# Optimization experiments

Measured on AMD Instinct MI355X. Metric: run time of the kernel, lower is better.

Reference implementation:

```python
import jax, jax.numpy as jnp
import numpy as np

PI_APPROX = 3.14  # the original module uses 3.14, not math.pi
FPS = 30.0        # hard-coded sampling rate in calc_hr_torch


def setup_inputs() -> dict:
    key = jax.random.key(0)
    x = jax.random.normal(key, (4096, 4096), dtype=jnp.float32)
    return {"x": x}


def reference(x) -> jnp.ndarray:
    test_n, sig_length = x.shape
    # mean-subtract each signal (over last dim)
    x = x - jnp.mean(x, axis=-1, keepdims=True)

    # custom_fft: DFT over dim 0 (size test_n), O(N^2) via trig matmuls
    N = test_n
    n = jnp.arange(N, dtype=jnp.float32)[:, None]  # [N,1]
    k = jnp.arange(N, dtype=jnp.float32)[None, :]  # [1,N]
    ang = (-2.0 * PI_APPROX / N) * (k * n)         # [N,N]
    real_part = jnp.matmul(jnp.cos(ang), x)        # [N, sig_length]
    imag_part = jnp.matmul(jnp.sin(ang), x)

    # custom_rfft: keep non-negative frequencies along dim 0
    half = N // 2 + 1 if N % 2 == 0 else (N + 1) // 2
    real_part = real_part[:half]
    imag_part = imag_part[:half]

    Ns = sig_length
    freq = jnp.arange(Ns, dtype=jnp.float32) / (Ns / FPS)  # [sig_length]
    amplitude = jnp.sqrt(real_part ** 2 + imag_part ** 2) / Ns  # [half, sig_length]
    hr_list = freq[jnp.argmax(amplitude, axis=-1)] * 60.0       # [half]
    return hr_list
```

## Files before the change

kernel.cpp:

```cpp
#include <hip/hip_runtime.h>
#include <cmath>

typedef _Float16 f16;
typedef _Float16 f16x8 __attribute__((ext_vector_type(8)));
typedef float f32x4 __attribute__((ext_vector_type(4)));
typedef unsigned long long u64;

#define M_OUT 2049
#define NDIM 4096
#define MPAD 2112
#define CW ((float)(-2.0 * 3.14 / 4096.0))

static const size_t WS_MEAN  = 0;
static const size_t WS_CELLS = 16384;
static const size_t WS_TBL   = 40960;
static const size_t A_ELEMS  = (size_t)MPAD * NDIM;
static const size_t X_ELEMS  = (size_t)NDIM * NDIM;
static const size_t WS_XTBL  = WS_TBL + 4 * A_ELEMS * sizeof(f16);
static const size_t WS_FULL_END = WS_XTBL + 2 * X_ELEMS * sizeof(f16);
static const size_t WS_MID_END  = WS_TBL + 4 * A_ELEMS * sizeof(f16);

#define AS1 __attribute__((address_space(1)))
#define AS3 __attribute__((address_space(3)))
__device__ __forceinline__ void async_copy16(const void* gsrc, void* ldst) {
    __builtin_amdgcn_global_load_lds((const AS1 unsigned int*)gsrc,
                                     (AS3 unsigned int*)ldst, 16, 0, 0);
}

__device__ __forceinline__ void split_f16(float v, f16& hi, f16& lo) {
    hi = (f16)v;
    lo = (f16)((v - (float)hi) * 64.0f);
}
__device__ __forceinline__ void split_raw(float v, f16& hi, f16& lo) {
    hi = (f16)v;
    lo = (f16)(v - (float)hi);
}

__global__ void mean_kernel(const float* __restrict__ x, float* __restrict__ meanv,
                            u64* __restrict__ cells) {
    if (blockIdx.x < 9) {
        int i = blockIdx.x * 256 + threadIdx.x;
        if (i < M_OUT) cells[i] = 0ull;
    }
    const int row = blockIdx.x;
    const float4* xr = (const float4*)(x + (size_t)row * NDIM);
    float s = 0.f;
    for (int i = threadIdx.x; i < NDIM / 4; i += 256) {
        float4 v = xr[i];
        s += (v.x + v.y) + (v.z + v.w);
    }
    for (int off = 32; off; off >>= 1) s += __shfl_down(s, off);
    __shared__ float ps[4];
    if ((threadIdx.x & 63) == 0) ps[threadIdx.x >> 6] = s;
    __syncthreads();
    if (threadIdx.x == 0) {
        float t = (ps[0] + ps[1]) + (ps[2] + ps[3]);
        meanv[row] = t * (1.0f / 4096.0f);
    }
}

__global__ __launch_bounds__(256) void nyq_partial(
    const float* __restrict__ x, const float* __restrict__ meanv,
    float* __restrict__ part)
{
    __shared__ float lc[256], ls[256];
    __shared__ float sC[128], sS[128];
    const int t = threadIdx.x;
    const int ks = blockIdx.y;
    const int kbase = ks * 256;
    sincosf(CW * (float)(2048 * (kbase + t)), &ls[t], &lc[t]);
    __syncthreads();
    const int col = blockIdx.x * 128 + (t & 127);
    const int kp  = t >> 7;
    float C = 0.f, S = 0.f;
    const float* xp = x + (size_t)(kbase + kp * 128) * NDIM + col;
    const float* mp = meanv + kbase + kp * 128;
    for (int i = 0; i < 128; ++i) {
        float v = xp[(size_t)i * NDIM] - mp[i];
        C = fmaf(lc[kp * 128 + i], v, C);
        S = fmaf(ls[kp * 128 + i], v, S);
    }
    if (kp) { sC[t - 128] = C; sS[t - 128] = S; }
    __syncthreads();
    if (!kp) {
        part[(size_t)ks * NDIM + col]            = C + sC[t];
        part[(size_t)(16 + ks) * NDIM + col]     = S + sS[t];
    }
}

__global__ __launch_bounds__(256) void nyq_reduce(
    const float* __restrict__ part, u64* __restrict__ cells)
{
    const int n = blockIdx.x * 256 + threadIdx.x;
    float C = 0.f, S = 0.f;
    for (int ks = 0; ks < 16; ++ks) {
        C += part[(size_t)ks * NDIM + n];
        S += part[(size_t)(16 + ks) * NDIM + n];
    }
    float a2 = C * C + S * S;
    u64 key = ((u64)__float_as_uint(a2) << 32) | (unsigned)(~n);
    for (int off = 1; off < 64; off <<= 1) {
        unsigned hi = (unsigned)(key >> 32), lo = (unsigned)key;
        unsigned ho = __shfl_xor(hi, off), lo2 = __shfl_xor(lo, off);
        u64 o = ((u64)ho << 32) | lo2;
        if (o > key) key = o;
    }
    if ((threadIdx.x & 63) == 0) atomicMax(cells + 2048, key);
}

__global__ void fill_tables_cm(const float* __restrict__ x, const float* __restrict__ meanv,
                               f16* __restrict__ atbl, f16* __restrict__ xtbl) {
    const int c = blockIdx.x;
    if (blockIdx.y < 9) {
        const int m = blockIdx.y * 256 + threadIdx.x;
        if (m >= MPAD) return;
        const bool valid = (m < M_OUT);
        f16x8 chv, clv, shv, slv;
        for (int j = 0; j < 8; ++j) {
            float cc = 0.f, ss = 0.f;
            if (valid) {
                int kk = c * 8 + j;
                float ang = CW * (float)(m * kk);
                sincosf(ang, &ss, &cc);
            }
            f16 h, l;
            split_raw(cc, h, l); chv[j] = h; clv[j] = l;
            split_raw(ss, h, l); shv[j] = h; slv[j] = l;
        }
        size_t idx = ((size_t)c * MPAD + m) * 8;
        *(f16x8*)(atbl + idx)                 = chv;
        *(f16x8*)(atbl + A_ELEMS + idx)       = clv;
        *(f16x8*)(atbl + 2 * A_ELEMS + idx)   = shv;
        *(f16x8*)(atbl + 3 * A_ELEMS + idx)   = slv;
    } else {
        const int n = (blockIdx.y - 9) * 256 + threadIdx.x;
        f16x8 hv, lv;
        for (int j = 0; j < 8; ++j) {
            int k = c * 8 + j;
            float v = x[(size_t)k * NDIM + n] - meanv[k];
            f16 h, l;
            split_raw(v, h, l);
            hv[j] = h; lv[j] = l;
        }
        size_t idx = ((size_t)c * NDIM + n) * 8;
        *(f16x8*)(xtbl + idx)           = hv;
        *(f16x8*)(xtbl + X_ELEMS + idx) = lv;
    }
}

__global__ __launch_bounds__(256, 4) void dft_gemm_cm(
    const f16* __restrict__ atbl, const f16* __restrict__ xtbl,
    u64* __restrict__ cells)
{
    __shared__ alignas(16) f16 sX[2][2][4][128][8];

    const int t = threadIdx.x;
    const int n0      = blockIdx.x * 128;
    const int rowBase = blockIdx.y * 64;

    const int lane = t & 63;
    const int w  = t >> 6;
    const int wm = w >> 1, wn = w & 1;
    const int q  = lane >> 4, ln = lane & 15;

    f32x4 aC[2][4], aS[2][4];
#pragma unroll
    for (int i = 0; i < 2; ++i)
#pragma unroll
        for (int j = 0; j < 4; ++j) {
            aC[i][j] = (f32x4){0.f, 0.f, 0.f, 0.f};
            aS[i][j] = (f32x4){0.f, 0.f, 0.f, 0.f};
        }

    const f16* aBase = atbl + ((size_t)q * MPAD + (rowBase + wm * 32 + ln)) * 8;

    const int xq0 = w >> 1, xh = w & 1;
    const int xq1 = xq0 + 2;
    const f16* xG0 = xtbl + ((size_t)xq0 * NDIM + n0 + xh * 64 + lane) * 8;
    const f16* xG1 = xtbl + ((size_t)xq1 * NDIM + n0 + xh * 64 + lane) * 8;
    const f16* xG2 = xG0 + X_ELEMS;
    const f16* xG3 = xG1 + X_ELEMS;

    auto loadA = [&](f16x8 (&dst)[2][4], int kc) {
#pragma unroll
        for (int tm = 0; tm < 2; ++tm)
#pragma unroll
            for (int tb = 0; tb < 4; ++tb)
                dst[tm][tb] = *(const f16x8*)(aBase + (size_t)tb * A_ELEMS
                              + ((size_t)kc * MPAD + tm * 16) * 8);
    };

    auto stageX = [&](int buf, int kc) {
        const size_t kadv = (size_t)kc * NDIM * 8;
        async_copy16(xG0 + kadv, &sX[buf][0][xq0][xh * 64][0]);
        async_copy16(xG1 + kadv, &sX[buf][0][xq1][xh * 64][0]);
        async_copy16(xG2 + kadv, &sX[buf][1][xq0][xh * 64][0]);
        async_copy16(xG3 + kadv, &sX[buf][1][xq1][xh * 64][0]);
    };

    auto compute = [&](f16x8 (&A)[2][4], int buf) {
        f16x8 bh[4], bl[4];
#pragma unroll
        for (int tn = 0; tn < 4; ++tn) {
            int nl = wn * 64 + tn * 16 + ln;
            bh[tn] = *(const f16x8*)&sX[buf][0][q][nl][0];
            bl[tn] = *(const f16x8*)&sX[buf][1][q][nl][0];
        }
        __builtin_amdgcn_s_setprio(1);
#pragma unroll
        for (int tm = 0; tm < 2; ++tm)
#pragma unroll
            for (int tn = 0; tn < 4; ++tn) {
                aC[tm][tn] = __builtin_amdgcn_mfma_f32_16x16x32_f16(A[tm][0], bh[tn], aC[tm][tn], 0, 0, 0);
                aC[tm][tn] = __builtin_amdgcn_mfma_f32_16x16x32_f16(A[tm][0], bl[tn], aC[tm][tn], 0, 0, 0);
                aC[tm][tn] = __builtin_amdgcn_mfma_f32_16x16x32_f16(A[tm][1], bh[tn], aC[tm][tn], 0, 0, 0);
                aS[tm][tn] = __builtin_amdgcn_mfma_f32_16x16x32_f16(A[tm][2], bh[tn], aS[tm][tn], 0, 0, 0);
                aS[tm][tn] = __builtin_amdgcn_mfma_f32_16x16x32_f16(A[tm][2], bl[tn], aS[tm][tn], 0, 0, 0);
                aS[tm][tn] = __builtin_amdgcn_mfma_f32_16x16x32_f16(A[tm][3], bh[tn], aS[tm][tn], 0, 0, 0);
            }
        __builtin_amdgcn_s_setprio(0);
    };

    f16x8 Aa[2][4];
    int cur = 0;

    stageX(0, 0);

    for (int kc = 0; kc < 512; kc += 4) {
        __syncthreads();
        if (kc + 4 < 512) stageX(cur ^ 1, kc + 4);
        loadA(Aa, kc);
        compute(Aa, cur);
        cur ^= 1;
    }

#pragma unroll
    for (int tm = 0; tm < 2; ++tm) {
#pragma unroll
        for (int r = 0; r < 4; ++r) {
            u64 best = 0ull;
#pragma unroll
            for (int tn = 0; tn < 4; ++tn) {
                float C = aC[tm][tn][r];
                float S = aS[tm][tn][r];
                float a2 = C * C + S * S;
                int col = n0 + wn * 64 + tn * 16 + ln;
                u64 key = ((u64)__float_as_uint(a2) << 32) | (unsigned)(~col);
                if (key > best) best = key;
            }
            for (int off = 1; off < 16; off <<= 1) {
                unsigned hi = (unsigned)(best >> 32), lo = (unsigned)best;
                unsigned ho = __shfl_xor(hi, off);
                unsigned lo2 = __shfl_xor(lo, off);
                u64 o = ((u64)ho << 32) | lo2;
                if (o > best) best = o;
            }
            if (ln == 0) {
                int grow = rowBase + wm * 32 + tm * 16 + q * 4 + r;
                if (grow < M_OUT) atomicMax(cells + grow, best);
            }
        }
    }
}

__global__ void fill_tables_rm(f16* __restrict__ tbl) {
    long long g = (long long)blockIdx.x * 256 + threadIdx.x;
    if (g >= (long long)(MPAD * 512)) return;
    int m  = (int)(g >> 9);
    int kq = ((int)g & 511) * 8;
    bool valid = (m < M_OUT);
    f16x8 chv, clv, shv, slv;
    for (int j = 0; j < 8; ++j) {
        float c = 0.f, s = 0.f;
        if (valid) {
            int kk = kq + j;
            float ang = CW * (float)(m * kk);
            sincosf(ang, &s, &c);
        }
        f16 h, l;
        split_f16(c, h, l); chv[j] = h; clv[j] = l;
        split_f16(s, h, l); shv[j] = h; slv[j] = l;
    }
    size_t idx = (size_t)m * NDIM + kq;
    *(f16x8*)(tbl + idx)               = chv;
    *(f16x8*)(tbl + A_ELEMS + idx)     = clv;
    *(f16x8*)(tbl + 2 * A_ELEMS + idx) = shv;
    *(f16x8*)(tbl + 3 * A_ELEMS + idx) = slv;
}

#define PK 40
__global__ __launch_bounds__(256, 2) void dft_gemm_fb(
    const float* __restrict__ x, const float* __restrict__ meanv,
    const f16* __restrict__ tbl, int useTbl,
    u64* __restrict__ cells)
{
    __shared__ alignas(16) f16 Ach[64][PK];
    __shared__ alignas(16) f16 Acl[64][PK];
    __shared__ alignas(16) f16 Ash[64][PK];
    __shared__ alignas(16) f16 Asl[64][PK];
    __shared__ alignas(16) f16 Xh[128][PK];
    __shared__ alignas(16) f16 Xl[128][PK];

    const int t = threadIdx.x;
    const int n0      = blockIdx.x * 128;
    const int rowBase = blockIdx.y * 64;

    const int am  = t >> 2;
    const int akq = (t & 3) * 8;
    const int xn  = t & 127;
    const int xkh = (t >> 7) * 16;

    const int lane = t & 63;
    const int w  = t >> 6;
    const int wm = w >> 1, wn = w & 1;
    const int q  = lane >> 4, ln = lane & 15;

    f32x4 aC0[2][4], aC1[2][4], aS0[2][4], aS1[2][4];
    for (int i = 0; i < 2; ++i)
        for (int j = 0; j < 4; ++j) {
            aC0[i][j] = (f32x4){0.f, 0.f, 0.f, 0.f};
            aC1[i][j] = (f32x4){0.f, 0.f, 0.f, 0.f};
            aS0[i][j] = (f32x4){0.f, 0.f, 0.f, 0.f};
            aS1[i][j] = (f32x4){0.f, 0.f, 0.f, 0.f};
        }

    const int arow = rowBase + am;
    const bool avalid = (arow < M_OUT);

    for (int k0 = 0; k0 < NDIM; k0 += 32) {
        __syncthreads();
        if (useTbl) {
            size_t idx = (size_t)arow * NDIM + k0 + akq;
            *(f16x8*)&Ach[am][akq] = *(const f16x8*)(tbl + idx);
            *(f16x8*)&Acl[am][akq] = *(const f16x8*)(tbl + A_ELEMS + idx);
            *(f16x8*)&Ash[am][akq] = *(const f16x8*)(tbl + 2 * A_ELEMS + idx);
            *(f16x8*)&Asl[am][akq] = *(const f16x8*)(tbl + 3 * A_ELEMS + idx);
        } else {
            f16x8 chv, clv, shv, slv;
            for (int j = 0; j < 8; ++j) {
                float c = 0.f, s = 0.f;
                if (avalid) {
                    int kk = k0 + akq + j;
                    float ang = CW * (float)(arow * kk);
                    sincosf(ang, &s, &c);
                }
                f16 h, l;
                split_f16(c, h, l); chv[j] = h; clv[j] = l;
                split_f16(s, h, l); shv[j] = h; slv[j] = l;
            }
            *(f16x8*)&Ach[am][akq] = chv;
            *(f16x8*)&Acl[am][akq] = clv;
            *(f16x8*)&Ash[am][akq] = shv;
            *(f16x8*)&Asl[am][akq] = slv;
        }
        {
            const float* xp = x + (size_t)(k0 + xkh) * NDIM + n0 + xn;
            f16x8 h0, h1, l0, l1;
            for (int r = 0; r < 16; ++r) {
                float v = xp[(size_t)r * NDIM] - meanv[k0 + xkh + r];
                f16 hi, lo;
                split_f16(v, hi, lo);
                if (r < 8) { h0[r] = hi; l0[r] = lo; }
                else       { h1[r - 8] = hi; l1[r - 8] = lo; }
            }
            *(f16x8*)&Xh[xn][xkh]     = h0;
            *(f16x8*)&Xh[xn][xkh + 8] = h1;
            *(f16x8*)&Xl[xn][xkh]     = l0;
            *(f16x8*)&Xl[xn][xkh + 8] = l1;
        }
        __syncthreads();
        f16x8 fch[2], fcl[2], fsh[2], fsl[2], bh[4], bl[4];
        for (int tm = 0; tm < 2; ++tm) {
            int ml = wm * 32 + tm * 16 + ln;
            fch[tm] = *(const f16x8*)&Ach[ml][q * 8];
            fcl[tm] = *(const f16x8*)&Acl[ml][q * 8];
            fsh[tm] = *(const f16x8*)&Ash[ml][q * 8];
            fsl[tm] = *(const f16x8*)&Asl[ml][q * 8];
        }
        for (int tn = 0; tn < 4; ++tn) {
            int nl = wn * 64 + tn * 16 + ln;
            bh[tn] = *(const f16x8*)&Xh[nl][q * 8];
            bl[tn] = *(const f16x8*)&Xl[nl][q * 8];
        }
        for (int tm = 0; tm < 2; ++tm)
            for (int tn = 0; tn < 4; ++tn) {
                aC0[tm][tn] = __builtin_amdgcn_mfma_f32_16x16x32_f16(fch[tm], bh[tn], aC0[tm][tn], 0, 0, 0);
                aC1[tm][tn] = __builtin_amdgcn_mfma_f32_16x16x32_f16(fch[tm], bl[tn], aC1[tm][tn], 0, 0, 0);
                aC1[tm][tn] = __builtin_amdgcn_mfma_f32_16x16x32_f16(fcl[tm], bh[tn], aC1[tm][tn], 0, 0, 0);
                aS0[tm][tn] = __builtin_amdgcn_mfma_f32_16x16x32_f16(fsh[tm], bh[tn], aS0[tm][tn], 0, 0, 0);
                aS1[tm][tn] = __builtin_amdgcn_mfma_f32_16x16x32_f16(fsh[tm], bl[tn], aS1[tm][tn], 0, 0, 0);
                aS1[tm][tn] = __builtin_amdgcn_mfma_f32_16x16x32_f16(fsl[tm], bh[tn], aS1[tm][tn], 0, 0, 0);
            }
    }

    const float inv64 = 0.015625f;
    for (int tm = 0; tm < 2; ++tm) {
        for (int r = 0; r < 4; ++r) {
            u64 best = 0ull;
            for (int tn = 0; tn < 4; ++tn) {
                float C = aC0[tm][tn][r] + aC1[tm][tn][r] * inv64;
                float S = aS0[tm][tn][r] + aS1[tm][tn][r] * inv64;
                float a2 = C * C + S * S;
                int col = n0 + wn * 64 + tn * 16 + ln;
                u64 key = ((u64)__float_as_uint(a2) << 32) | (unsigned)(~col);
                if (key > best) best = key;
            }
            for (int off = 1; off < 16; off <<= 1) {
                unsigned hi = (unsigned)(best >> 32), lo = (unsigned)best;
                unsigned ho = __shfl_xor(hi, off);
                unsigned lo2 = __shfl_xor(lo, off);
                u64 o = ((u64)ho << 32) | lo2;
                if (o > best) best = o;
            }
            if (ln == 0) {
                int grow = rowBase + wm * 32 + tm * 16 + q * 4 + r;
                if (grow < M_OUT) atomicMax(cells + grow, best);
            }
        }
    }
}

__global__ void out_kernel(const u64* __restrict__ cells, float* __restrict__ out) {
    int i = blockIdx.x * 256 + threadIdx.x;
    if (i < M_OUT) {
        unsigned col = ~(unsigned)(cells[i] & 0xFFFFFFFFull);
        float freq = (float)col / (4096.0f / 30.0f);
        out[i] = freq * 60.0f;
    }
}

extern "C" void kernel_launch(void* const* d_in, const int* in_sizes, int n_in,
                              void* d_out, int out_size, void* d_ws, size_t ws_size,
                              hipStream_t stream) {
    const float* x = (const float*)d_in[0];
    char* ws = (char*)d_ws;
    float* meanv = (float*)(ws + WS_MEAN);
    u64*   cells = (u64*)(ws + WS_CELLS);
    f16*   atbl  = (f16*)(ws + WS_TBL);
    f16*   xtbl  = (f16*)(ws + WS_XTBL);
    float* nyqp  = (float*)(ws + WS_TBL);
    float* out   = (float*)d_out;

    hipLaunchKernelGGL(mean_kernel, dim3(NDIM), dim3(256), 0, stream, x, meanv, cells);

    if (ws_size >= WS_FULL_END) {
        hipLaunchKernelGGL(nyq_partial, dim3(32, 16), dim3(256), 0, stream, x, meanv, nyqp);
        hipLaunchKernelGGL(nyq_reduce, dim3(16), dim3(256), 0, stream, nyqp, cells);
        hipLaunchKernelGGL(fill_tables_cm, dim3(512, 25), dim3(256), 0, stream,
                           x, meanv, atbl, xtbl);
        hipLaunchKernelGGL(dft_gemm_cm, dim3(32, 32), dim3(256), 0, stream, atbl, xtbl, cells);
    } else if (ws_size >= WS_MID_END) {
        hipLaunchKernelGGL(fill_tables_rm, dim3(4224), dim3(256), 0, stream, atbl);
        hipLaunchKernelGGL(dft_gemm_fb, dim3(32, 33), dim3(256), 0, stream,
                           x, meanv, atbl, 1, cells);
    } else {
        hipLaunchKernelGGL(dft_gemm_fb, dim3(32, 33), dim3(256), 0, stream,
                           x, meanv, atbl, 0, cells);
    }
    hipLaunchKernelGGL(out_kernel, dim3((M_OUT + 255) / 256), dim3(256), 0, stream, cells, out);
}
```

Measured before the change: 530.7 us.

## Widen GEMM N-tile to 256 and replace syncthreads with explicit waitcnt pipelining

Doubles the column tile per block of the DFT GEMM from 128 to 256, giving each wave 8 N-subtiles so each A fragment loaded from global memory is reused twice as often. It also replaces __syncthreads with a raw s_barrier plus sched_barriers and a partial vmcnt wait, so the next X tile's async copies can stay in flight while compute runs. The cost is doubled accumulator registers (launch bounds drop to 2 blocks per SM), twice the LDS, and half as many blocks in the grid. The hand-written waitcnt relies on the exact count of outstanding loads to stay correct.

Result: faster. 451.7 us (-14.9%).

```diff
diff --git a/kernel.cpp b/kernel.cpp
--- a/kernel.cpp
+++ b/kernel.cpp
@@ -148,14 +148,14 @@
     }
 }
 
-__global__ __launch_bounds__(256, 4) void dft_gemm_cm(
+__global__ __launch_bounds__(256, 2) void dft_gemm_cm(
     const f16* __restrict__ atbl, const f16* __restrict__ xtbl,
     u64* __restrict__ cells)
 {
-    __shared__ alignas(16) f16 sX[2][2][4][128][8];
+    __shared__ alignas(16) f16 sX[2][2][4][256][8];
 
     const int t = threadIdx.x;
-    const int n0      = blockIdx.x * 128;
+    const int n0      = blockIdx.x * 256;
     const int rowBase = blockIdx.y * 64;
 
     const int lane = t & 63;
@@ -163,23 +163,17 @@
     const int wm = w >> 1, wn = w & 1;
     const int q  = lane >> 4, ln = lane & 15;
 
-    f32x4 aC[2][4], aS[2][4];
+    f32x4 aC[2][8], aS[2][8];
 #pragma unroll
     for (int i = 0; i < 2; ++i)
 #pragma unroll
-        for (int j = 0; j < 4; ++j) {
+        for (int j = 0; j < 8; ++j) {
             aC[i][j] = (f32x4){0.f, 0.f, 0.f, 0.f};
             aS[i][j] = (f32x4){0.f, 0.f, 0.f, 0.f};
         }
 
     const f16* aBase = atbl + ((size_t)q * MPAD + (rowBase + wm * 32 + ln)) * 8;
-
-    const int xq0 = w >> 1, xh = w & 1;
-    const int xq1 = xq0 + 2;
-    const f16* xG0 = xtbl + ((size_t)xq0 * NDIM + n0 + xh * 64 + lane) * 8;
-    const f16* xG1 = xtbl + ((size_t)xq1 * NDIM + n0 + xh * 64 + lane) * 8;
-    const f16* xG2 = xG0 + X_ELEMS;
-    const f16* xG3 = xG1 + X_ELEMS;
+    const f16* xBase = xtbl + (size_t)(n0 + w * 64 + lane) * 8;
 
     auto loadA = [&](f16x8 (&dst)[2][4], int kc) {
 #pragma unroll
@@ -191,33 +185,32 @@
     };
 
     auto stageX = [&](int buf, int kc) {
-        const size_t kadv = (size_t)kc * NDIM * 8;
-        async_copy16(xG0 + kadv, &sX[buf][0][xq0][xh * 64][0]);
-        async_copy16(xG1 + kadv, &sX[buf][0][xq1][xh * 64][0]);
-        async_copy16(xG2 + kadv, &sX[buf][1][xq0][xh * 64][0]);
-        async_copy16(xG3 + kadv, &sX[buf][1][xq1][xh * 64][0]);
+        const f16* src = xBase + (size_t)kc * (NDIM * 8);
+#pragma unroll
+        for (int tb = 0; tb < 2; ++tb)
+#pragma unroll
+            for (int p = 0; p < 4; ++p)
+                async_copy16(src + (size_t)tb * X_ELEMS + (size_t)p * (NDIM * 8),
+                             &sX[buf][tb][p][w * 64][0]);
     };
 
     auto compute = [&](f16x8 (&A)[2][4], int buf) {
-        f16x8 bh[4], bl[4];
-#pragma unroll
-        for (int tn = 0; tn < 4; ++tn) {
-            int nl = wn * 64 + tn * 16 + ln;
-            bh[tn] = *(const f16x8*)&sX[buf][0][q][nl][0];
-            bl[tn] = *(const f16x8*)&sX[buf][1][q][nl][0];
-        }
         __builtin_amdgcn_s_setprio(1);
 #pragma unroll
-        for (int tm = 0; tm < 2; ++tm)
-#pragma unroll
-            for (int tn = 0; tn < 4; ++tn) {
-                aC[tm][tn] = __builtin_amdgcn_mfma_f32_16x16x32_f16(A[tm][0], bh[tn], aC[tm][tn], 0, 0, 0);
-                aC[tm][tn] = __builtin_amdgcn_mfma_f32_16x16x32_f16(A[tm][0], bl[tn], aC[tm][tn], 0, 0, 0);
-                aC[tm][tn] = __builtin_amdgcn_mfma_f32_16x16x32_f16(A[tm][1], bh[tn], aC[tm][tn], 0, 0, 0);
-                aS[tm][tn] = __builtin_amdgcn_mfma_f32_16x16x32_f16(A[tm][2], bh[tn], aS[tm][tn], 0, 0, 0);
-                aS[tm][tn] = __builtin_amdgcn_mfma_f32_16x16x32_f16(A[tm][2], bl[tn], aS[tm][tn], 0, 0, 0);
-                aS[tm][tn] = __builtin_amdgcn_mfma_f32_16x16x32_f16(A[tm][3], bh[tn], aS[tm][tn], 0, 0, 0);
-            }
+        for (int tn = 0; tn < 8; ++tn) {
+            int nl = wn * 128 + tn * 16 + ln;
+            f16x8 bh = *(const f16x8*)&sX[buf][0][q][nl][0];
+            f16x8 bl = *(const f16x8*)&sX[buf][1][q][nl][0];
+#pragma unroll
+            for (int tm = 0; tm < 2; ++tm) {
+                aC[tm][tn] = __builtin_amdgcn_mfma_f32_16x16x32_f16(A[tm][0], bh, aC[tm][tn], 0, 0, 0);
+                aC[tm][tn] = __builtin_amdgcn_mfma_f32_16x16x32_f16(A[tm][0], bl, aC[tm][tn], 0, 0, 0);
+                aC[tm][tn] = __builtin_amdgcn_mfma_f32_16x16x32_f16(A[tm][1], bh, aC[tm][tn], 0, 0, 0);
+                aS[tm][tn] = __builtin_amdgcn_mfma_f32_16x16x32_f16(A[tm][2], bh, aS[tm][tn], 0, 0, 0);
+                aS[tm][tn] = __builtin_amdgcn_mfma_f32_16x16x32_f16(A[tm][2], bl, aS[tm][tn], 0, 0, 0);
+                aS[tm][tn] = __builtin_amdgcn_mfma_f32_16x16x32_f16(A[tm][3], bh, aS[tm][tn], 0, 0, 0);
+            }
+        }
         __builtin_amdgcn_s_setprio(0);
     };
 
@@ -227,9 +220,18 @@
     stageX(0, 0);
 
     for (int kc = 0; kc < 512; kc += 4) {
-        __syncthreads();
-        if (kc + 4 < 512) stageX(cur ^ 1, kc + 4);
+        __builtin_amdgcn_s_barrier();
+        __builtin_amdgcn_sched_barrier(0);
         loadA(Aa, kc);
+        __builtin_amdgcn_sched_barrier(0);
+        if (kc + 4 < 512) {
+            stageX(cur ^ 1, kc + 4);
+            __builtin_amdgcn_sched_barrier(0);
+            asm volatile("s_waitcnt vmcnt(8)" ::: "memory");
+        } else {
+            asm volatile("s_waitcnt vmcnt(0)" ::: "memory");
+        }
+        __builtin_amdgcn_sched_barrier(0);
         compute(Aa, cur);
         cur ^= 1;
     }
@@ -240,11 +242,11 @@
         for (int r = 0; r < 4; ++r) {
             u64 best = 0ull;
 #pragma unroll
-            for (int tn = 0; tn < 4; ++tn) {
+            for (int tn = 0; tn < 8; ++tn) {
                 float C = aC[tm][tn][r];
                 float S = aS[tm][tn][r];
                 float a2 = C * C + S * S;
-                int col = n0 + wn * 64 + tn * 16 + ln;
+                int col = n0 + wn * 128 + tn * 16 + ln;
                 u64 key = ((u64)__float_as_uint(a2) << 32) | (unsigned)(~col);
                 if (key > best) best = key;
             }
@@ -448,7 +450,7 @@
         hipLaunchKernelGGL(nyq_reduce, dim3(16), dim3(256), 0, stream, nyqp, cells);
         hipLaunchKernelGGL(fill_tables_cm, dim3(512, 25), dim3(256), 0, stream,
                            x, meanv, atbl, xtbl);
-        hipLaunchKernelGGL(dft_gemm_cm, dim3(32, 32), dim3(256), 0, stream, atbl, xtbl, cells);
+        hipLaunchKernelGGL(dft_gemm_cm, dim3(16, 32), dim3(256), 0, stream, atbl, xtbl, cells);
     } else if (ws_size >= WS_MID_END) {
         hipLaunchKernelGGL(fill_tables_rm, dim3(4224), dim3(256), 0, stream, atbl);
         hipLaunchKernelGGL(dft_gemm_fb, dim3(32, 33), dim3(256), 0, stream,
```
